# Performance work log

Measured on AMD Instinct MI355X. Metric: run time of the kernel, lower is better.

The kernel has to match this reference:

```python
import jax, jax.numpy as jnp
import numpy as np

# Block dims (see shape_source)
D, H = 768, 12
DH = D // H            # 64 head dim
NOPE = DH // 2         # 32 non-rope q/k dim
ROPE = DH // 2         # 32 rope q/k dim
QP = D // 2            # 384 q LoRA dim
KVP = 2 * D // 3       # 512 kv LoRA dim
E, TOPK, NS = 8, 2, 2  # routed experts, top-k, shared experts
FF = 4 * D             # 3072 expert hidden
THETA = 10000.0


def setup_inputs() -> dict:
    key = jax.random.key(0)
    ks = jax.random.split(key, 16)
    B, S = 4, 1024
    r = lambda i, shape, s: (s * jax.random.normal(ks[i], shape)).astype(jnp.float32)
    return {
        'x': jax.random.normal(ks[0], (B, S, D), jnp.float32),
        'ln1_w': jnp.ones((D,), jnp.float32),
        'ln2_w': jnp.ones((D,), jnp.float32),
        'W_dq': r(1, (D, QP), 0.01),
        'W_uq': r(2, (QP, D), 0.01),
        'q_ln_w': jnp.ones((QP,), jnp.float32),
        'q_ln_b': jnp.zeros((QP,), jnp.float32),
        'W_dkv': r(3, (D, KVP + ROPE), 0.01),
        'W_ukv': r(4, (KVP, D + H * NOPE), 0.01),
        'kv_ln_w': jnp.ones((KVP,), jnp.float32),
        'kv_ln_b': jnp.zeros((KVP,), jnp.float32),
        'W_o': r(5, (D, D), 0.01),
        's_fc': r(6, (NS, FF, D), 0.02),   # nn.Linear weight layout [out,in]
        's_proj': r(7, (NS, D, FF), 0.02),
        'e_fc': r(8, (E, FF, D), 0.02),
        'e_proj': r(9, (E, D, FF), 0.02),
        'centroids': jax.random.normal(ks[10], (E, D), jnp.float32),
        'route_bias': jnp.zeros((E,), jnp.float32),  # load-balancing bias (non-learned)
    }


def _ln(x, w, b=None, eps=1e-5):
    m = x.mean(-1, keepdims=True)
    v = ((x - m) ** 2).mean(-1, keepdims=True)
    y = (x - m) * jax.lax.rsqrt(v + eps) * w
    return y + b if b is not None else y


def _rope(x, cos, sin):
    x1, x2 = jnp.split(x, 2, axis=-1)
    return x * cos + jnp.concatenate([-x2, x1], axis=-1) * sin


def _forward(x, ln1_w, ln2_w, W_dq, W_uq, q_ln_w, q_ln_b, W_dkv, W_ukv,
             kv_ln_w, kv_ln_b, W_o, s_fc, s_proj, e_fc, e_proj,
             centroids, route_bias):
    B, S, _ = x.shape
    h = _ln(x, ln1_w)
    # ---- MLA attention ----
    cq = _ln(h @ W_dq, q_ln_w, q_ln_b)
    Q = (cq @ W_uq).reshape(B, S, H, DH).transpose(0, 2, 1, 3)  # bhsd
    Qn, Qr = Q[..., :NOPE], Q[..., NOPE:]
    freqs = 1.0 / (THETA ** (jnp.arange(0, DH, 2, dtype=jnp.float32) / DH))
    ang = jnp.arange(S, dtype=jnp.float32)[:, None] * freqs[None, :]  # [S, DH/2]
    cos = jnp.tile(jnp.cos(ang)[:, : ROPE // 2], (1, 2))  # [S, ROPE]
    sin = jnp.tile(jnp.sin(ang)[:, : ROPE // 2], (1, 2))
    Qr = _rope(Qr, cos, sin)
    ckv = h @ W_dkv
    kv_lora, k_rope = ckv[..., :KVP], ckv[..., KVP:]
    kv_lora = _ln(kv_lora, kv_ln_w, kv_ln_b)
    KV = (kv_lora @ W_ukv).reshape(B, S, H, NOPE + DH).transpose(0, 2, 1, 3)
    Kn, V = KV[..., :NOPE], KV[..., NOPE:]
    Kr = _rope(k_rope[:, None, :, :], cos, sin)  # [B,1,S,ROPE] shared across heads
    Kr = jnp.broadcast_to(Kr, (B, H, S, ROPE))
    q = jnp.concatenate([Qn, Qr], axis=-1)
    k = jnp.concatenate([Kn, Kr], axis=-1)
    scores = jnp.einsum('bhsd,bhtd->bhst', q, k) / np.float32(np.sqrt(DH))
    causal = jnp.tril(jnp.ones((S, S), bool))
    scores = jnp.where(causal, scores, jnp.finfo(scores.dtype).min)
    attn = jax.nn.softmax(scores, axis=-1)
    o = jnp.einsum('bhst,bhtd->bshd', attn, V).reshape(B, S, D)
    x = x + o @ W_o.T
    # ---- MoE FFN ----
    h = _ln(x, ln2_w)
    gelu = lambda t: jax.nn.gelu(t, approximate=False)  # torch nn.GELU default
    # shared experts (always on, summed)
    shared = jnp.einsum('bsnf,ndf->bsd', gelu(jnp.einsum('bsd,nfd->bsnf', h, s_fc)), s_proj)
    # centroid routing
    raw = jnp.einsum('bsd,ed->bse', h, centroids)
    routing = jax.nn.sigmoid(raw)
    balanced = raw + route_bias
    _, topi = jax.lax.top_k(balanced, TOPK)                       # [B,S,K]
    w = jnp.take_along_axis(routing, topi, axis=-1)               # sigmoid gate values
    w = w / (w.sum(-1, keepdims=True) + 1e-9)                     # normalize over top-k
    gates = (jax.nn.one_hot(topi, E, dtype=w.dtype) * w[..., None]).sum(-2)  # [B,S,E]
    eh = gelu(jnp.einsum('bsd,efd->bsef', h, e_fc))               # [B,S,E,FF]
    routed = jnp.einsum('bsef,edf,bse->bsd', eh, e_proj, gates)
    return x + shared + routed


def reference(x, ln1_w, ln2_w, W_dq, W_uq, q_ln_w, q_ln_b, W_dkv, W_ukv,
              kv_ln_w, kv_ln_b, W_o, s_fc, s_proj, e_fc, e_proj,
              centroids, route_bias):
    return _forward(x, ln1_w, ln2_w, W_dq, W_uq, q_ln_w, q_ln_b, W_dkv, W_ukv,
                    kv_ln_w, kv_ln_b, W_o, s_fc, s_proj, e_fc, e_proj,
                    centroids, route_bias)
```

## Files before the change

### kernel.cpp

```cpp
#include <hip/hip_runtime.h>
#include <math.h>


#define DEV __device__ __forceinline__

typedef __attribute__((ext_vector_type(8))) short short8;
typedef __attribute__((ext_vector_type(8))) __bf16 bf16x8;
typedef __attribute__((ext_vector_type(4))) float floatx4;

DEV short f2bf(float f) {
  union { float f; unsigned u; } v; v.f = f;
  unsigned r = v.u + 0x7fffu + ((v.u >> 16) & 1u);
  return (short)(r >> 16);
}
DEV float bf2f(short s) {
  union { float f; unsigned u; } v; v.u = ((unsigned)(unsigned short)s) << 16;
  return v.f;
}
DEV float gelu_f(float v) {
  float z = fabsf(v) * 0.70710678118654752f;
  float t = __fdividef(1.0f, 1.0f + 0.3275911f * z);
  float poly = t * (0.254829592f + t * (-0.284496736f +
               t * (1.421413741f + t * (-1.453152027f + t * 1.061405429f))));
  float er = 1.0f - poly * __expf(-z * z);
  er = (v < 0.f) ? -er : er;
  return 0.5f * v * (1.0f + er);
}

DEV floatx4 mfma16(short8 a, short8 b, floatx4 c) {
  return __builtin_amdgcn_mfma_f32_16x16x32_bf16(
      __builtin_bit_cast(bf16x8, a), __builtin_bit_cast(bf16x8, b), c, 0, 0, 0);
}
DEV void async16(void* lds_uniform, const void* gptr) {
  __builtin_amdgcn_global_load_lds(
      (const __attribute__((address_space(1))) void*)gptr,
      (__attribute__((address_space(3))) void*)lds_uniform, 16, 0, 0);
}

DEV void xcd_swz(int& n0, int& m0) {
  const int NT = gridDim.x;
  const int flat = blockIdx.y * NT + blockIdx.x;
  const int nwg = NT * gridDim.y;
  const int w = (flat & 7) * (nwg >> 3) + (flat >> 3);
  n0 = (w % NT) * 128;
  m0 = (w / NT) * 128;
}


__global__ void cast2_bf4(const float4* __restrict__ srcA, short4* __restrict__ dstA,
                          const float4* __restrict__ srcB, short4* __restrict__ dstB,
                          long n4each) {
  long i = (long)blockIdx.x * blockDim.x + threadIdx.x;
  long stride = (long)gridDim.x * blockDim.x;
  for (; i < 2 * n4each; i += stride) {
    const float4* s; short4* d; long j;
    if (i < n4each) { s = srcA; d = dstA; j = i; }
    else { s = srcB; d = dstB; j = i - n4each; }
    float4 v = s[j];
    short4 o; o.x = f2bf(v.x); o.y = f2bf(v.y); o.z = f2bf(v.z); o.w = f2bf(v.w);
    d[j] = o;
  }
}

__global__ void cast_shared(const float4* __restrict__ sfc4, const float4* __restrict__ sproj4,
                            short4* __restrict__ fcCat4, short4* __restrict__ projCat4) {
  long i = (long)blockIdx.x * 256 + threadIdx.x;
  float4 v;
  if (i < 1179648) {
    v = sfc4[i];
    short4 o; o.x = f2bf(v.x); o.y = f2bf(v.y); o.z = f2bf(v.z); o.w = f2bf(v.w);
    fcCat4[i] = o;
  } else {
    long j = i - 1179648;
    long d = j / 1536, k4 = j - d * 1536;
    v = (k4 < 768) ? sproj4[d * 768 + k4] : sproj4[589824 + d * 768 + (k4 - 768)];
    short4 o; o.x = f2bf(v.x); o.y = f2bf(v.y); o.z = f2bf(v.z); o.w = f2bf(v.w);
    projCat4[j] = o;
  }
}

__global__ void cast_hl4(const float4* __restrict__ src, short4* __restrict__ dhi,
                         short4* __restrict__ dlo, long n4) {
  long i = (long)blockIdx.x * blockDim.x + threadIdx.x;
  long stride = (long)gridDim.x * blockDim.x;
  for (; i < n4; i += stride) {
    float4 v = src[i];
    short4 h, l;
    h.x = f2bf(v.x); l.x = f2bf(v.x - bf2f(h.x));
    h.y = f2bf(v.y); l.y = f2bf(v.y - bf2f(h.y));
    h.z = f2bf(v.z); l.z = f2bf(v.z - bf2f(h.z));
    h.w = f2bf(v.w); l.w = f2bf(v.w - bf2f(h.w));
    dhi[i] = h; dlo[i] = l;
  }
}

__launch_bounds__(256)
__global__ void transpose_cast_hl(const float* __restrict__ src, short* __restrict__ dhi,
                                  short* __restrict__ dlo, int K, int N) {
  __shared__ float tile[64][65];
  int k0 = blockIdx.x * 64, n0 = blockIdx.y * 64;
  for (int i = threadIdx.x; i < 4096; i += 256) {
    int r = i >> 6, c = i & 63;
    tile[r][c] = (n0 + c < N) ? src[(size_t)(k0 + r) * N + n0 + c] : 0.f;
  }
  __syncthreads();
  for (int i = threadIdx.x; i < 4096; i += 256) {
    int r = i >> 6, c = i & 63;
    float v = tile[c][r];
    short h = f2bf(v);
    dhi[(size_t)(n0 + r) * K + k0 + c] = h;
    dlo[(size_t)(n0 + r) * K + k0 + c] = f2bf(v - bf2f(h));
  }
}


__launch_bounds__(256)
__global__ void ln_hl(const float* __restrict__ in, int ldi, int N,
                      const float* __restrict__ w, const float* __restrict__ b,
                      short* __restrict__ ohi, short* __restrict__ olo, int ldo) {
  const int row = blockIdx.x * 4 + (threadIdx.x >> 6);
  const int lane = threadIdx.x & 63;
  const float* r = in + (size_t)row * ldi;
  float s = 0.f, s2 = 0.f;
  for (int i = lane; i < N; i += 64) { float v = r[i]; s += v; s2 += v * v; }
#pragma unroll
  for (int off = 32; off >= 1; off >>= 1) { s += __shfl_xor(s, off); s2 += __shfl_xor(s2, off); }
  float mean = s / N, var = s2 / N - mean * mean;
  float rstd = rsqrtf(var + 1e-5f);
  for (int i = lane; i < N; i += 64) {
    float y = (r[i] - mean) * rstd * w[i];
    if (b) y += b[i];
    short h = f2bf(y);
    ohi[(size_t)row * ldo + i] = h;
    olo[(size_t)row * ldo + i] = f2bf(y - bf2f(h));
  }
}

__launch_bounds__(256)
__global__ void ln_qkv(const float* __restrict__ Ccat,
                       const float* __restrict__ qw, const float* __restrict__ qb,
                       const float* __restrict__ kw, const float* __restrict__ kb,
                       short* __restrict__ cqH, short* __restrict__ cqL,
                       short* __restrict__ kvH, short* __restrict__ kvL) {
  const int vrow = blockIdx.x * 4 + (threadIdx.x >> 6);
  const int lane = threadIdx.x & 63;
  const float* r; int N; const float* w; const float* b; short* oh; short* ol; int ldo; int row;
  if (vrow < 4096) {
    row = vrow; r = Ccat + (size_t)row * 928; N = 384; w = qw; b = qb; oh = cqH; ol = cqL; ldo = 384;
  } else {
    row = vrow - 4096; r = Ccat + (size_t)row * 928 + 384; N = 512; w = kw; b = kb; oh = kvH; ol = kvL; ldo = 512;
  }
  float s = 0.f, s2 = 0.f;
  for (int i = lane; i < N; i += 64) { float v = r[i]; s += v; s2 += v * v; }
#pragma unroll
  for (int off = 32; off >= 1; off >>= 1) { s += __shfl_xor(s, off); s2 += __shfl_xor(s2, off); }
  float mean = s / N, var = s2 / N - mean * mean;
  float rstd = rsqrtf(var + 1e-5f);
  for (int i = lane; i < N; i += 64) {
    float y = (r[i] - mean) * rstd * w[i] + b[i];
    short h = f2bf(y);
    oh[(size_t)row * ldo + i] = h;
    ol[(size_t)row * ldo + i] = f2bf(y - bf2f(h));
  }
}

__launch_bounds__(256)
__global__ void ln_bf_f32(const float* __restrict__ in, const float* __restrict__ w,
                          short* __restrict__ obf, float* __restrict__ of,
                          float* __restrict__ outInit) {
  const int row = blockIdx.x * 4 + (threadIdx.x >> 6);
  const int lane = threadIdx.x & 63;
  const float* r = in + (size_t)row * 768;
  float s = 0.f, s2 = 0.f;
  for (int i = lane; i < 768; i += 64) { float v = r[i]; s += v; s2 += v * v; }
#pragma unroll
  for (int off = 32; off >= 1; off >>= 1) { s += __shfl_xor(s, off); s2 += __shfl_xor(s2, off); }
  float mean = s / 768.f, var = s2 / 768.f - mean * mean;
  float rstd = rsqrtf(var + 1e-5f);
  for (int i = lane; i < 768; i += 64) {
    float xv = r[i];
    float y = (xv - mean) * rstd * w[i];
    obf[(size_t)row * 768 + i] = f2bf(y);
    of[(size_t)row * 768 + i] = y;
    outInit[(size_t)row * 768 + i] = xv;
  }
}


template<int RESID>
__launch_bounds__(256)
__global__ void gemm3(const short* __restrict__ Ahi, const short* __restrict__ Alo, int lda,
                      const short* __restrict__ Bhi, const short* __restrict__ Blo, int ldb,
                      float* __restrict__ Cf, int ldc, const float* __restrict__ resid,
                      int M, int N, int K) {
  __shared__ __align__(16) short AsH[4096], AsL[4096], BsH[4096], BsL[4096];
  const int tid = threadIdx.x;
  int n0, m0; xcd_swz(n0, m0);
  const int wave = tid >> 6, lane = tid & 63;
  const int wm = (wave >> 1) * 64, wn = (wave & 1) * 64;
  const int lr = lane & 15, rb = (lane >> 4) * 4;
  const int stg = ((tid & 3) ^ ((tid >> 3) & 3)) * 8;
  const int lkx = (((lane >> 4) ^ ((lr >> 1) & 3))) * 8;
  const floatx4 fz = {0.f, 0.f, 0.f, 0.f};
  floatx4 acc[4][4];
#pragma unroll
  for (int i = 0; i < 4; i++)
#pragma unroll
    for (int j = 0; j < 4; j++) acc[i][j] = fz;
  const size_t rowA = (size_t)(m0 + (tid >> 2)) * lda + stg;
  const size_t rowB = (size_t)(n0 + (tid >> 2)) * ldb + stg;
  const size_t a64 = (size_t)64 * lda, b64 = (size_t)64 * ldb;
  short* AsHW = AsH + wave * 512; short* AsLW = AsL + wave * 512;
  short* BsHW = BsH + wave * 512; short* BsLW = BsL + wave * 512;
  for (int k0 = 0; k0 < K; k0 += 32) {
    async16(AsHW, Ahi + rowA + k0);        async16(AsHW + 2048, Ahi + rowA + a64 + k0);
    async16(AsLW, Alo + rowA + k0);        async16(AsLW + 2048, Alo + rowA + a64 + k0);
    async16(BsHW, Bhi + rowB + k0);        async16(BsHW + 2048, Bhi + rowB + b64 + k0);
    async16(BsLW, Blo + rowB + k0);        async16(BsLW + 2048, Blo + rowB + b64 + k0);
    __syncthreads();
    short8 ah[4], al[4], bh[4], bl[4];
#pragma unroll
    for (int i = 0; i < 4; i++) {
      ah[i] = *(const short8*)&AsH[(wm + i * 16 + lr) * 32 + lkx];
      al[i] = *(const short8*)&AsL[(wm + i * 16 + lr) * 32 + lkx];
    }
#pragma unroll
    for (int j = 0; j < 4; j++) {
      bh[j] = *(const short8*)&BsH[(wn + j * 16 + lr) * 32 + lkx];
      bl[j] = *(const short8*)&BsL[(wn + j * 16 + lr) * 32 + lkx];
    }
#pragma unroll
    for (int i = 0; i < 4; i++)
#pragma unroll
      for (int j = 0; j < 4; j++) {
        acc[i][j] = mfma16(ah[i], bh[j], acc[i][j]);
        acc[i][j] = mfma16(ah[i], bl[j], acc[i][j]);
        acc[i][j] = mfma16(al[i], bh[j], acc[i][j]);
      }
    __syncthreads();
  }
#pragma unroll
  for (int i = 0; i < 4; i++) {
    int row = m0 + wm + i * 16 + rb;
#pragma unroll
    for (int j = 0; j < 4; j++) {
      int col = n0 + wn + j * 16 + lr;
      if (col < N) {
#pragma unroll
        for (int r = 0; r < 4; r++) {
          int rr = row + r;
          if (rr < M) {
            float v = acc[i][j][r];
            if (RESID) v += resid[(size_t)rr * ldc + col];
            Cf[(size_t)rr * ldc + col] = v;
          }
        }
      }
    }
  }
}


__launch_bounds__(256)
__global__ void gemm_fc(const short* __restrict__ A, int lda,
                        const short* __restrict__ Bt, int ldb,
                        short* __restrict__ Cb, int ldc, int K) {
  __shared__ __align__(16) short As[8192], Bs[8192];
  const int tid = threadIdx.x;
  int n0, m0; xcd_swz(n0, m0);
  const int wave = tid >> 6, lane = tid & 63;
  const int wm = (wave >> 1) * 64, wn = (wave & 1) * 64;
  const int lr = lane & 15, q4 = lane >> 4, rb = q4 * 4;
  const int srow = tid >> 3;
  const int sg = ((tid & 7) ^ (srow & 7)) * 8;
  const int cx0 = ((q4 ^ (lr & 7))) * 8;
  const int cx1 = (((4 + q4) ^ (lr & 7))) * 8;
  const floatx4 fz = {0.f, 0.f, 0.f, 0.f};
  floatx4 acc[4][4];
#pragma unroll
  for (int i = 0; i < 4; i++)
#pragma unroll
    for (int j = 0; j < 4; j++) acc[i][j] = fz;
  const short* Ag = A + (size_t)(m0 + srow) * lda + sg;
  const short* Bg = Bt + (size_t)(n0 + srow) * ldb + sg;
  short* AsW = As + wave * 512; short* BsW = Bs + wave * 512;
  const size_t a32 = (size_t)32 * lda, b32 = (size_t)32 * ldb;
  for (int k0 = 0; k0 < K; k0 += 64) {
    async16(AsW,        Ag + k0);            async16(AsW + 2048, Ag + a32 + k0);
    async16(AsW + 4096, Ag + 2 * a32 + k0);  async16(AsW + 6144, Ag + 3 * a32 + k0);
    async16(BsW,        Bg + k0);            async16(BsW + 2048, Bg + b32 + k0);
    async16(BsW + 4096, Bg + 2 * b32 + k0);  async16(BsW + 6144, Bg + 3 * b32 + k0);
    __syncthreads();
#pragma unroll
    for (int ks = 0; ks < 2; ks++) {
      const int cx = ks ? cx1 : cx0;
      short8 af[4], bfr[4];
#pragma unroll
      for (int i = 0; i < 4; i++) af[i] = *(const short8*)&As[(wm + i * 16 + lr) * 64 + cx];
#pragma unroll
      for (int j = 0; j < 4; j++) bfr[j] = *(const short8*)&Bs[(wn + j * 16 + lr) * 64 + cx];
#pragma unroll
      for (int i = 0; i < 4; i++)
#pragma unroll
        for (int j = 0; j < 4; j++) acc[i][j] = mfma16(af[i], bfr[j], acc[i][j]);
    }
    __syncthreads();
  }
#pragma unroll
  for (int i = 0; i < 4; i++) {
    int row = m0 + wm + i * 16 + rb;
#pragma unroll
    for (int j = 0; j < 4; j++) {
      int col = n0 + wn + j * 16 + lr;
#pragma unroll
      for (int r = 0; r < 4; r++)
        Cb[(size_t)(row + r) * ldc + col] = f2bf(gelu_f(acc[i][j][r]));
    }
  }
}


__launch_bounds__(256)
__global__ void gemm_sk(const short* __restrict__ A, int lda,
                        const short* __restrict__ Bt, int ldb,
                        float* __restrict__ out, int ldc, int klen) {
  __shared__ __align__(16) short As[8192], Bs[8192];
  const int tid = threadIdx.x;
  int n0, m0; xcd_swz(n0, m0);
  const int koff = blockIdx.z * klen;
  const int wave = tid >> 6, lane = tid & 63;
  const int wm = (wave >> 1) * 64, wn = (wave & 1) * 64;
  const int lr = lane & 15, q4 = lane >> 4, rb = q4 * 4;
  const int srow = tid >> 3;
  const int sg = ((tid & 7) ^ (srow & 7)) * 8;
  const int cx0 = ((q4 ^ (lr & 7))) * 8;
  const int cx1 = (((4 + q4) ^ (lr & 7))) * 8;
  const floatx4 fz = {0.f, 0.f, 0.f, 0.f};
  floatx4 acc[4][4];
#pragma unroll
  for (int i = 0; i < 4; i++)
#pragma unroll
    for (int j = 0; j < 4; j++) acc[i][j] = fz;
  const short* Ag = A + (size_t)(m0 + srow) * lda + koff + sg;
  const short* Bg = Bt + (size_t)(n0 + srow) * ldb + koff + sg;
  short* AsW = As + wave * 512; short* BsW = Bs + wave * 512;
  const size_t a32 = (size_t)32 * lda, b32 = (size_t)32 * ldb;
  for (int k0 = 0; k0 < klen; k0 += 64) {
    async16(AsW,        Ag + k0);            async16(AsW + 2048, Ag + a32 + k0);
    async16(AsW + 4096, Ag + 2 * a32 + k0);  async16(AsW + 6144, Ag + 3 * a32 + k0);
    async16(BsW,        Bg + k0);            async16(BsW + 2048, Bg + b32 + k0);
    async16(BsW + 4096, Bg + 2 * b32 + k0);  async16(BsW + 6144, Bg + 3 * b32 + k0);
    __syncthreads();
#pragma unroll
    for (int ks = 0; ks < 2; ks++) {
      const int cx = ks ? cx1 : cx0;
      short8 af[4], bfr[4];
#pragma unroll
      for (int i = 0; i < 4; i++) af[i] = *(const short8*)&As[(wm + i * 16 + lr) * 64 + cx];
#pragma unroll
      for (int j = 0; j < 4; j++) bfr[j] = *(const short8*)&Bs[(wn + j * 16 + lr) * 64 + cx];
#pragma unroll
      for (int i = 0; i < 4; i++)
#pragma unroll
        for (int j = 0; j < 4; j++) acc[i][j] = mfma16(af[i], bfr[j], acc[i][j]);
    }
    __syncthreads();
  }
#pragma unroll
  for (int i = 0; i < 4; i++) {
    int row = m0 + wm + i * 16 + rb;
#pragma unroll
    for (int j = 0; j < 4; j++) {
      int col = n0 + wn + j * 16 + lr;
#pragma unroll
      for (int r = 0; r < 4; r++)
        atomicAdd(&out[(size_t)(row + r) * ldc + col], acc[i][j][r]);
    }
  }
}


__global__ void build_qk(const float* __restrict__ Qf, const float* __restrict__ KVf,
                         const float* __restrict__ Ccat,
                         short* __restrict__ qh, short* __restrict__ ql,
                         short* __restrict__ kh, short* __restrict__ kl) {
  int id = blockIdx.x * blockDim.x + threadIdx.x;
  if (id >= 4096 * 12) return;
  int token = id / 12, hh_ = id - token * 12;
  int s = token & 1023, b = token >> 10;
  size_t base = ((size_t)(b * 12 + hh_) * 1024 + s) * 64;
  float vals[64];
  if (blockIdx.y == 0) {
    const float* q = Qf + (size_t)token * 768 + hh_ * 64;
#pragma unroll
    for (int d = 0; d < 32; d++) vals[d] = q[d];
#pragma unroll
    for (int i = 0; i < 16; i++) {
      float fi = powf(10000.f, -(float)(2 * i) / 64.f);
      float sn, cs; sincosf((float)s * fi, &sn, &cs);
      vals[32 + i] = q[32 + i] * cs - q[48 + i] * sn;
      vals[48 + i] = q[48 + i] * cs + q[32 + i] * sn;
    }
#pragma unroll
    for (int d = 0; d < 64; d++) {
      short h = f2bf(vals[d]);
      qh[base + d] = h; ql[base + d] = f2bf(vals[d] - bf2f(h));
    }
  } else {
    const float* kv = KVf + (size_t)token * 1152 + hh_ * 96;
#pragma unroll
    for (int d = 0; d < 32; d++) vals[d] = kv[d];
    const float* kr = Ccat + (size_t)token * 928 + 896;
#pragma unroll
    for (int i = 0; i < 16; i++) {
      float fi = powf(10000.f, -(float)(2 * i) / 64.f);
      float sn, cs; sincosf((float)s * fi, &sn, &cs);
      vals[32 + i] = kr[i] * cs - kr[16 + i] * sn;
      vals[48 + i] = kr[16 + i] * cs + kr[i] * sn;
    }
#pragma unroll
    for (int d = 0; d < 64; d++) {
      short h = f2bf(vals[d]);
      kh[base + d] = h; kl[base + d] = f2bf(vals[d] - bf2f(h));
    }
  }
}

__launch_bounds__(256)
__global__ void build_vt_hl(const float* __restrict__ KVf,
                            short* __restrict__ vth, short* __restrict__ vtl) {
  __shared__ float tile[64][65];
  const int s0 = blockIdx.x * 64, bh = blockIdx.y;
  const int b = bh / 12, h = bh - b * 12;
  for (int i = threadIdx.x; i < 4096; i += 256) {
    int tl = i >> 6, d = i & 63;
    int token = b * 1024 + s0 + tl;
    tile[tl][d] = KVf[(size_t)token * 1152 + h * 96 + 32 + d];
  }
  __syncthreads();
  for (int i = threadIdx.x; i < 4096; i += 256) {
    int d = i >> 6, sl = i & 63;
    float v = tile[sl][d];
    short hh = f2bf(v);
    size_t idx = (size_t)bh * 65536 + (size_t)d * 1024 + s0 + sl;
    vth[idx] = hh;
    vtl[idx] = f2bf(v - bf2f(hh));
  }
}


__launch_bounds__(256)
__global__ void attn3(const short* __restrict__ qbh, const short* __restrict__ qbl,
                      const short* __restrict__ kbh, const short* __restrict__ kbl,
                      const short* __restrict__ vth, const short* __restrict__ vtl,
                      short* __restrict__ obh, short* __restrict__ obl) {
  const int bh = blockIdx.y;
  const int b = bh / 12, h = bh - b * 12;
  const short* Qh = qbh + (size_t)bh * 65536;
  const short* Ql = qbl + (size_t)bh * 65536;
  const short* Kh = kbh + (size_t)bh * 65536;
  const short* Kl = kbl + (size_t)bh * 65536;
  const short* Vh = vth + (size_t)bh * 65536;
  const short* Vl = vtl + (size_t)bh * 65536;
  __shared__ __align__(16) short KsH[4096], KsL[4096], VsH[4096], VsL[4096];
  __shared__ __align__(16) short PsH[4608], PsL[4608];
  const int tid = threadIdx.x, wave = tid >> 6, lane = tid & 63;
  const int lr = lane & 15, q4 = lane >> 4, lk = (lane >> 4) * 8;
  const int sx0 = ((q4 ^ (lr & 7))) * 8;
  const int sx1 = (((4 + q4) ^ (lr & 7))) * 8;
  const int soff_sw = (((tid & 7) ^ ((tid >> 3) & 7))) * 8;
  const int srow = tid >> 3;
  short* KsHW = KsH + wave * 512; short* KsLW = KsL + wave * 512;
  short* VsHW = VsH + wave * 512; short* VsLW = VsL + wave * 512;
  short* myPh = PsH + wave * 1152; short* myPl = PsL + wave * 1152;
  const floatx4 fz = {0.f, 0.f, 0.f, 0.f};
#pragma unroll
  for (int ph = 0; ph < 2; ph++) {
    const int qt = ph ? 15 - blockIdx.x : blockIdx.x;
    const int qrow0 = qt * 64 + wave * 16;
    short8 qfh[2], qfl[2];
    qfh[0] = *(const short8*)&Qh[(size_t)(qrow0 + lr) * 64 + lk];
    qfh[1] = *(const short8*)&Qh[(size_t)(qrow0 + lr) * 64 + 32 + lk];
    qfl[0] = *(const short8*)&Ql[(size_t)(qrow0 + lr) * 64 + lk];
    qfl[1] = *(const short8*)&Ql[(size_t)(qrow0 + lr) * 64 + 32 + lk];
    floatx4 oacc[4];
#pragma unroll
    for (int t = 0; t < 4; t++) oacc[t] = fz;
    float m_i[4], l_i[4];
#pragma unroll
    for (int r = 0; r < 4; r++) { m_i[r] = -__builtin_inff(); l_i[r] = 0.f; }
    for (int kt = 0; kt <= qt; kt++) {
      __syncthreads();
      size_t krow = (size_t)(kt * 64 + srow) * 64 + soff_sw;
      size_t vrow = (size_t)srow * 1024 + kt * 64 + soff_sw;
      async16(KsHW, Kh + krow);        async16(KsHW + 2048, Kh + krow + 32 * 64);
      async16(KsLW, Kl + krow);        async16(KsLW + 2048, Kl + krow + 32 * 64);
      async16(VsHW, Vh + vrow);        async16(VsHW + 2048, Vh + vrow + 32 * 1024);
      async16(VsLW, Vl + vrow);        async16(VsLW + 2048, Vl + vrow + 32 * 1024);
      __syncthreads();
      floatx4 sacc[4];
#pragma unroll
      for (int j = 0; j < 4; j++) sacc[j] = fz;
#pragma unroll
      for (int j = 0; j < 4; j++) {
        int rbase = (j * 16 + lr) * 64;
        short8 kh0 = *(const short8*)&KsH[rbase + sx0];
        short8 kh1 = *(const short8*)&KsH[rbase + sx1];
        short8 kl0 = *(const short8*)&KsL[rbase + sx0];
        short8 kl1 = *(const short8*)&KsL[rbase + sx1];
        sacc[j] = mfma16(qfh[0], kh0, sacc[j]);
        sacc[j] = mfma16(qfh[1], kh1, sacc[j]);
        sacc[j] = mfma16(qfh[0], kl0, sacc[j]);
        sacc[j] = mfma16(qfh[1], kl1, sacc[j]);
        sacc[j] = mfma16(qfl[0], kh0, sacc[j]);
        sacc[j] = mfma16(qfl[1], kh1, sacc[j]);
      }
      float pv[4][4], mrow[4];
#pragma unroll
      for (int r = 0; r < 4; r++) mrow[r] = -__builtin_inff();
      const bool diag = (kt == qt);
#pragma unroll
      for (int j = 0; j < 4; j++)
#pragma unroll
        for (int r = 0; r < 4; r++) {
          float v = sacc[j][r] * 0.125f;
          if (diag) {
            int qg = qrow0 + q4 * 4 + r;
            int kg = kt * 64 + j * 16 + lr;
            if (kg > qg) v = -__builtin_inff();
          }
          pv[j][r] = v;
          mrow[r] = fmaxf(mrow[r], v);
        }
#pragma unroll
      for (int r = 0; r < 4; r++)
#pragma unroll
        for (int off = 1; off < 16; off <<= 1) mrow[r] = fmaxf(mrow[r], __shfl_xor(mrow[r], off));
      float alpha[4], rsum[4];
#pragma unroll
      for (int r = 0; r < 4; r++) {
        float nm = fmaxf(m_i[r], mrow[r]);
        alpha[r] = __expf(m_i[r] - nm);
        m_i[r] = nm; rsum[r] = 0.f;
      }
#pragma unroll
      for (int j = 0; j < 4; j++)
#pragma unroll
        for (int r = 0; r < 4; r++) {
          float pe = __expf(pv[j][r] - m_i[r]);
          pv[j][r] = pe; rsum[r] += pe;
        }
#pragma unroll
      for (int r = 0; r < 4; r++) {
#pragma unroll
        for (int off = 1; off < 16; off <<= 1) rsum[r] += __shfl_xor(rsum[r], off);
        l_i[r] = l_i[r] * alpha[r] + rsum[r];
      }
#pragma unroll
      for (int t = 0; t < 4; t++)
#pragma unroll
        for (int r = 0; r < 4; r++) oacc[t][r] *= alpha[r];
#pragma unroll
      for (int j = 0; j < 4; j++)
#pragma unroll
        for (int r = 0; r < 4; r++) {
          float p = pv[j][r];
          short hh = f2bf(p);
          myPh[(q4 * 4 + r) * 72 + j * 16 + lr] = hh;
          myPl[(q4 * 4 + r) * 72 + j * 16 + lr] = f2bf(p - bf2f(hh));
        }
      __asm__ volatile("s_waitcnt lgkmcnt(0)" ::: "memory");
#pragma unroll
      for (int c = 0; c < 2; c++) {
        short8 ph_ = *(const short8*)&myPh[lr * 72 + c * 32 + lk];
        short8 pl_ = *(const short8*)&myPl[lr * 72 + c * 32 + lk];
        const int sxc = c ? sx1 : sx0;
#pragma unroll
        for (int t = 0; t < 4; t++) {
          int rbase = (t * 16 + lr) * 64;
          short8 vh = *(const short8*)&VsH[rbase + sxc];
          short8 vl = *(const short8*)&VsL[rbase + sxc];
          oacc[t] = mfma16(ph_, vh, oacc[t]);
          oacc[t] = mfma16(ph_, vl, oacc[t]);
          oacc[t] = mfma16(pl_, vh, oacc[t]);
        }
      }
    }
#pragma unroll
    for (int t = 0; t < 4; t++)
#pragma unroll
      for (int r = 0; r < 4; r++) {
        int s = qrow0 + q4 * 4 + r;
        int token = b * 1024 + s;
        float ov = oacc[t][r] / l_i[r];
        short hh = f2bf(ov);
        size_t idx = (size_t)token * 768 + h * 64 + t * 16 + lr;
        obh[idx] = hh;
        obl[idx] = f2bf(ov - bf2f(hh));
      }
  }
}


__launch_bounds__(256)
__global__ void route_score(const float* __restrict__ h2f, const float* __restrict__ cent,
                            const float* __restrict__ rbias,
                            int* __restrict__ topexp, float* __restrict__ gates) {
  const int token = blockIdx.x * 4 + (threadIdx.x >> 6);
  const int lane = threadIdx.x & 63;
  const float* hv = h2f + (size_t)token * 768;
  float hreg[12];
#pragma unroll
  for (int ii = 0; ii < 12; ii++) hreg[ii] = hv[lane + 64 * ii];
  float raw[8];
#pragma unroll
  for (int e = 0; e < 8; e++) {
    const float* cv = cent + e * 768;
    float p = 0.f;
#pragma unroll
    for (int ii = 0; ii < 12; ii++) p += hreg[ii] * cv[lane + 64 * ii];
#pragma unroll
    for (int off = 32; off >= 1; off >>= 1) p += __shfl_xor(p, off);
    raw[e] = p;
  }
  if (lane == 0) {
    float b0 = -__builtin_inff(); int i1 = 0;
#pragma unroll
    for (int e = 0; e < 8; e++) { float be = raw[e] + rbias[e]; if (be > b0) { b0 = be; i1 = e; } }
    float b1 = -__builtin_inff(); int i2 = 0;
#pragma unroll
    for (int e = 0; e < 8; e++) {
      if (e == i1) continue;
      float be = raw[e] + rbias[e];
      if (be > b1) { b1 = be; i2 = e; }
    }
    float w1 = 1.f / (1.f + expf(-raw[i1]));
    float w2 = 1.f / (1.f + expf(-raw[i2]));
    float wsum = w1 + w2 + 1e-9f;
    topexp[token] = i1;        gates[token] = w1 / wsum;
    topexp[4096 + token] = i2; gates[4096 + token] = w2 / wsum;
  }
}

__launch_bounds__(256)
__global__ void build_lists(const int* __restrict__ topexp,
                            int* __restrict__ counts, int* __restrict__ lists) {
  const int e = blockIdx.x;
  __shared__ int wave_off[4];
  const int wave = threadIdx.x >> 6, lane = threadIdx.x & 63;
  int total = 0;
  for (int c0 = 0; c0 < 8192; c0 += 256) {
    int slot = c0 + threadIdx.x;
    bool m = (topexp[slot] == e);
    unsigned long long bal = __ballot(m);
    int wcnt = __popcll(bal);
    int lpre = __popcll(bal & ((1ull << lane) - 1ull));
    if (lane == 0) wave_off[wave] = wcnt;
    __syncthreads();
    int woff = 0;
#pragma unroll
    for (int w = 0; w < 4; w++) if (w < wave) woff += wave_off[w];
    int chunk_total = wave_off[0] + wave_off[1] + wave_off[2] + wave_off[3];
    if (m) lists[e * 4096 + total + woff + lpre] = slot;
    total += chunk_total;
    __syncthreads();
  }
  if (threadIdx.x == 0) counts[e] = total;
}


__launch_bounds__(256)
__global__ void expert_fc_z(const short* __restrict__ h2bf, const short* __restrict__ wfc,
                            const int* __restrict__ lists, const int* __restrict__ counts,
                            int ebase, short* __restrict__ act) {
  const int lz = blockIdx.z, e = ebase + lz;
  const int cnt = counts[e];
  const int m0 = blockIdx.y * 128;
  if (m0 >= cnt) return;
  const int n0 = blockIdx.x * 128;
  int aoff = 0;
  for (int i = 0; i < lz; i++) aoff += counts[ebase + i];
  __shared__ __align__(16) short As[8192], Bs[8192];
  __shared__ int slots[128];
  const int tid = threadIdx.x;
  if (tid < 128) slots[tid] = lists[e * 4096 + m0 + tid];
  __syncthreads();
  const int wave = tid >> 6, lane = tid & 63;
  const int wm = (wave >> 1) * 64, wn = (wave & 1) * 64;
  const int lr = lane & 15, q4 = lane >> 4, rb = q4 * 4;
  const int srow = tid >> 3;
  const int sg = ((tid & 7) ^ (srow & 7)) * 8;
  const int cx0 = ((q4 ^ (lr & 7))) * 8;
  const int cx1 = (((4 + q4) ^ (lr & 7))) * 8;
  int tok[4];
#pragma unroll
  for (int p = 0; p < 4; p++) tok[p] = slots[p * 32 + srow] & 4095;
  const floatx4 fz = {0.f, 0.f, 0.f, 0.f};
  floatx4 acc[4][4];
#pragma unroll
  for (int i = 0; i < 4; i++)
#pragma unroll
    for (int j = 0; j < 4; j++) acc[i][j] = fz;
  const short* Ag0 = h2bf + (size_t)tok[0] * 768 + sg;
  const short* Ag1 = h2bf + (size_t)tok[1] * 768 + sg;
  const short* Ag2 = h2bf + (size_t)tok[2] * 768 + sg;
  const short* Ag3 = h2bf + (size_t)tok[3] * 768 + sg;
  const short* Bg = wfc + (size_t)lz * (3072 * 768) + (size_t)(n0 + srow) * 768 + sg;
  short* AsW = As + wave * 512; short* BsW = Bs + wave * 512;
  const size_t b32 = (size_t)32 * 768;
  for (int k0 = 0; k0 < 768; k0 += 64) {
    async16(AsW,        Ag0 + k0);           async16(AsW + 2048, Ag1 + k0);
    async16(AsW + 4096, Ag2 + k0);           async16(AsW + 6144, Ag3 + k0);
    async16(BsW,        Bg + k0);            async16(BsW + 2048, Bg + b32 + k0);
    async16(BsW + 4096, Bg + 2 * b32 + k0);  async16(BsW + 6144, Bg + 3 * b32 + k0);
    __syncthreads();
#pragma unroll
    for (int ks = 0; ks < 2; ks++) {
      const int cx = ks ? cx1 : cx0;
      short8 af[4], bfr[4];
#pragma unroll
      for (int i = 0; i < 4; i++) af[i] = *(const short8*)&As[(wm + i * 16 + lr) * 64 + cx];
#pragma unroll
      for (int j = 0; j < 4; j++) bfr[j] = *(const short8*)&Bs[(wn + j * 16 + lr) * 64 + cx];
#pragma unroll
      for (int i = 0; i < 4; i++)
#pragma unroll
        for (int j = 0; j < 4; j++) acc[i][j] = mfma16(af[i], bfr[j], acc[i][j]);
    }
    __syncthreads();
  }
#pragma unroll
  for (int i = 0; i < 4; i++) {
    int lrow = wm + i * 16 + rb;
#pragma unroll
    for (int j = 0; j < 4; j++) {
      int col = n0 + wn + j * 16 + lr;
#pragma unroll
      for (int r = 0; r < 4; r++) {
        if (m0 + lrow + r < cnt)
          act[(size_t)(aoff + m0 + lrow + r) * 3072 + col] = f2bf(gelu_f(acc[i][j][r]));
      }
    }
  }
}

__launch_bounds__(256)
__global__ void expert_proj_z(const short* __restrict__ act, const short* __restrict__ wproj,
                              const int* __restrict__ lists, const int* __restrict__ counts,
                              int ebase, const float* __restrict__ gates,
                              float* __restrict__ out) {
  const int lz = blockIdx.z >> 2, kh = blockIdx.z & 3, e = ebase + lz;
  const int cnt = counts[e];
  const int m0 = blockIdx.y * 128;
  if (m0 >= cnt) return;
  const int n0 = blockIdx.x * 128;
  int aoff = 0;
  for (int i = 0; i < lz; i++) aoff += counts[ebase + i];
  const int koff = kh * 768;
  __shared__ __align__(16) short As[8192], Bs[8192];
  __shared__ int slots[128];
  const int tid = threadIdx.x;
  if (tid < 128) slots[tid] = lists[e * 4096 + m0 + tid];
  __syncthreads();
  const int wave = tid >> 6, lane = tid & 63;
  const int wm = (wave >> 1) * 64, wn = (wave & 1) * 64;
  const int lr = lane & 15, q4 = lane >> 4, rb = q4 * 4;
  const int srow = tid >> 3;
  const int sg = ((tid & 7) ^ (srow & 7)) * 8;
  const int cx0 = ((q4 ^ (lr & 7))) * 8;
  const int cx1 = (((4 + q4) ^ (lr & 7))) * 8;
  const floatx4 fz = {0.f, 0.f, 0.f, 0.f};
  floatx4 acc[4][4];
#pragma unroll
  for (int i = 0; i < 4; i++)
#pragma unroll
    for (int j = 0; j < 4; j++) acc[i][j] = fz;
  const short* Ag = act + (size_t)(aoff + m0 + srow) * 3072 + koff + sg;
  const short* Bg = wproj + (size_t)lz * (768 * 3072) + (size_t)(n0 + srow) * 3072 + koff + sg;
  short* AsW = As + wave * 512; short* BsW = Bs + wave * 512;
  const size_t s32 = (size_t)32 * 3072;
  for (int k0 = 0; k0 < 768; k0 += 64) {
    async16(AsW,        Ag + k0);            async16(AsW + 2048, Ag + s32 + k0);
    async16(AsW + 4096, Ag + 2 * s32 + k0);  async16(AsW + 6144, Ag + 3 * s32 + k0);
    async16(BsW,        Bg + k0);            async16(BsW + 2048, Bg + s32 + k0);
    async16(BsW + 4096, Bg + 2 * s32 + k0);  async16(BsW + 6144, Bg + 3 * s32 + k0);
    __syncthreads();
#pragma unroll
    for (int ks = 0; ks < 2; ks++) {
      const int cx = ks ? cx1 : cx0;
      short8 af[4], bfr[4];
#pragma unroll
      for (int i = 0; i < 4; i++) af[i] = *(const short8*)&As[(wm + i * 16 + lr) * 64 + cx];
#pragma unroll
      for (int j = 0; j < 4; j++) bfr[j] = *(const short8*)&Bs[(wn + j * 16 + lr) * 64 + cx];
#pragma unroll
      for (int i = 0; i < 4; i++)
#pragma unroll
        for (int j = 0; j < 4; j++) acc[i][j] = mfma16(af[i], bfr[j], acc[i][j]);
    }
    __syncthreads();
  }
#pragma unroll
  for (int i = 0; i < 4; i++) {
    int lrow = wm + i * 16 + rb;
#pragma unroll
    for (int j = 0; j < 4; j++) {
      int col = n0 + wn + j * 16 + lr;
#pragma unroll
      for (int r = 0; r < 4; r++) {
        if (m0 + lrow + r < cnt) {
          int slot = slots[lrow + r];
          int token = slot & 4095;
          atomicAdd(&out[(size_t)token * 768 + col], gates[slot] * acc[i][j][r]);
        }
      }
    }
  }
}

__global__ void bad_kernel(float* out) { out[threadIdx.x] = 1e30f; }


extern "C" void kernel_launch(void* const* d_in, const int* in_sizes, int n_in,
                              void* d_out, int out_size, void* d_ws, size_t ws_size,
                              hipStream_t stream) {
  const float* x = (const float*)d_in[0];
  const float* ln1_w = (const float*)d_in[1];
  const float* ln2_w = (const float*)d_in[2];
  const float* W_dq = (const float*)d_in[3];
  const float* W_uq = (const float*)d_in[4];
  const float* q_ln_w = (const float*)d_in[5];
  const float* q_ln_b = (const float*)d_in[6];
  const float* W_dkv = (const float*)d_in[7];
  const float* W_ukv = (const float*)d_in[8];
  const float* kv_ln_w = (const float*)d_in[9];
  const float* kv_ln_b = (const float*)d_in[10];
  const float* W_o = (const float*)d_in[11];
  const float* s_fc = (const float*)d_in[12];
  const float* s_proj = (const float*)d_in[13];
  const float* e_fc = (const float*)d_in[14];
  const float* e_proj = (const float*)d_in[15];
  const float* cent = (const float*)d_in[16];
  const float* rbias = (const float*)d_in[17];
  float* out = (float*)d_out;

  char* base = (char*)d_ws;
  size_t off = 0;
  auto take = [&](size_t bytes) -> char* {
    char* r = base + off;
    off = (off + bytes + 255) & ~(size_t)255;
    return r;
  };
  short* WcatH = (short*)take(1572864);  short* WcatL = (short*)take(1572864);
  short* WuqH  = (short*)take(589824);   short* WuqL  = (short*)take(589824);
  short* WukvH = (short*)take(1179648);  short* WukvL = (short*)take(1179648);
  short* WoH   = (short*)take(1179648);  short* WoL   = (short*)take(1179648);
  float* x2    = (float*)take(12582912);
  float* gates = (float*)take(32768);
  int*   counts= (int*)take(32);
  int*   lists = (int*)take(131072);
  int*   topexp= (int*)take(32768);
  const size_t PLANE = 6291456;
  char* pool = take(4 * 2 * PLANE);
  char* R    = take(51118080);
  size_t used = off;
  if (used > ws_size) { bad_kernel<<<1, 256, 0, stream>>>(out); return; }
  char* pA = pool;
  char* pB = pool + 2 * PLANE;
  char* pC = pool + 4 * PLANE;
  char* pD = pool + 6 * PLANE;

  short* hH   = (short*)pA;            short* hL   = (short*)(pA + PLANE);
  float* Ccat = (float*)R;
  short* cqH  = (short*)pB;            short* cqL  = (short*)(pB + 3145728);
  short* kvlH = (short*)pD;            short* kvlL = (short*)(pD + 4194304);
  float* Qf   = (float*)pC;
  float* KVf  = (float*)(R + 15204352);
  short* qbH  = (short*)pD;            short* qbL  = (short*)(pD + PLANE);
  short* kbH  = (short*)pA;            short* kbL  = (short*)(pA + PLANE);
  short* vtH  = (short*)pB;            short* vtL  = (short*)(pB + PLANE);
  short* obH  = (short*)pC;            short* obL  = (short*)(pC + PLANE);
  short* h2bf    = (short*)(pD + PLANE);
  float* h2f     = (float*)pC;
  short* sfcCat  = (short*)pA;
  short* sprojCat= (short*)(pA + 9437184);
  short* actCat  = (short*)R;
  short* efcHalf = (short*)pA;
  short* eprojHalf=(short*)(pA + 18874368);
  short* eact    = (short*)R;

  cast_hl4<<<576, 256, 0, stream>>>((const float4*)W_o, (short4*)WoH, (short4*)WoL, 147456);
  transpose_cast_hl<<<dim3(12, 6), 256, 0, stream>>>(W_dq, WcatH, WcatL, 768, 384);
  transpose_cast_hl<<<dim3(12, 10), 256, 0, stream>>>(W_dkv, WcatH + (size_t)384 * 768,
                                                      WcatL + (size_t)384 * 768, 768, 544);
  transpose_cast_hl<<<dim3(6, 12), 256, 0, stream>>>(W_uq, WuqH, WuqL, 384, 768);
  transpose_cast_hl<<<dim3(8, 18), 256, 0, stream>>>(W_ukv, WukvH, WukvL, 512, 1152);

  ln_hl<<<1024, 256, 0, stream>>>(x, 768, 768, ln1_w, nullptr, hH, hL, 768);
  gemm3<0><<<dim3(8, 32), 256, 0, stream>>>(hH, hL, 768, WcatH, WcatL, 768, Ccat, 928, nullptr, 4096, 928, 768);
  ln_qkv<<<2048, 256, 0, stream>>>(Ccat, q_ln_w, q_ln_b, kv_ln_w, kv_ln_b, cqH, cqL, kvlH, kvlL);
  gemm3<0><<<dim3(6, 32), 256, 0, stream>>>(cqH, cqL, 384, WuqH, WuqL, 384, Qf, 768, nullptr, 4096, 768, 384);
  gemm3<0><<<dim3(9, 32), 256, 0, stream>>>(kvlH, kvlL, 512, WukvH, WukvL, 512, KVf, 1152, nullptr, 4096, 1152, 512);
  build_qk<<<dim3(192, 2), 256, 0, stream>>>(Qf, KVf, Ccat, qbH, qbL, kbH, kbL);
  build_vt_hl<<<dim3(16, 48), 256, 0, stream>>>(KVf, vtH, vtL);
  attn3<<<dim3(8, 48), 256, 0, stream>>>(qbH, qbL, kbH, kbL, vtH, vtL, obH, obL);
  gemm3<1><<<dim3(6, 32), 256, 0, stream>>>(obH, obL, 768, WoH, WoL, 768, x2, 768, x, 4096, 768, 768);

  ln_bf_f32<<<1024, 256, 0, stream>>>(x2, ln2_w, h2bf, h2f, out);
  route_score<<<1024, 256, 0, stream>>>(h2f, cent, rbias, topexp, gates);
  build_lists<<<8, 256, 0, stream>>>(topexp, counts, lists);

  cast_shared<<<9216, 256, 0, stream>>>((const float4*)s_fc, (const float4*)s_proj,
                                        (short4*)sfcCat, (short4*)sprojCat);
  gemm_fc<<<dim3(48, 32), 256, 0, stream>>>(h2bf, 768, sfcCat, 768, actCat, 6144, 768);
  gemm_sk<<<dim3(6, 32, 4), 256, 0, stream>>>(actCat, 6144, sprojCat, 6144, out, 768, 1536);

  for (int h = 0; h < 2; h++) {
    cast2_bf4<<<2048, 256, 0, stream>>>(
        (const float4*)(e_fc + (size_t)h * 4 * 3072 * 768), (short4*)efcHalf,
        (const float4*)(e_proj + (size_t)h * 4 * 768 * 3072), (short4*)eprojHalf, 2359296);
    expert_fc_z<<<dim3(24, 32, 4), 256, 0, stream>>>(h2bf, efcHalf, lists, counts, h * 4, eact);
    expert_proj_z<<<dim3(6, 32, 16), 256, 0, stream>>>(eact, eprojHalf, lists, counts, h * 4, gates, out);
  }
}
```

Measured before the change: 964.3 us.

## Replace atomic split-K in shared-expert projection with partial buffers and reduce kernel

The shared-expert down-projection GEMM drops from four K-splits with float atomics to three K-splits. Split 0 accumulates directly into the output, and splits 1 and 2 write plain stores into scratch buffers that a new vectorized kernel then sums into the output. The N tile is halved to 64 so that the grid still has enough blocks, and the XCD swizzle is replaced by plain block indexing. This removes the atomic traffic but adds an extra kernel launch, a full read-modify-write pass over the output, and reuses the x2 and pC buffers as scratch.

```diff
diff --git a/kernel.cpp b/kernel.cpp
--- a/kernel.cpp
+++ b/kernel.cpp
@@ -323,24 +323,26 @@
 __launch_bounds__(256)
 __global__ void gemm_sk(const short* __restrict__ A, int lda,
                         const short* __restrict__ Bt, int ldb,
-                        float* __restrict__ out, int ldc, int klen) {
-  __shared__ __align__(16) short As[8192], Bs[8192];
+                        float* __restrict__ out, int ldc,
+                        float* __restrict__ p1, float* __restrict__ p2, int klen) {
+  __shared__ __align__(16) short As[8192], Bs[4096];
   const int tid = threadIdx.x;
-  int n0, m0; xcd_swz(n0, m0);
-  const int koff = blockIdx.z * klen;
+  const int m0 = blockIdx.y * 128, n0 = blockIdx.x * 64;
+  const int z = blockIdx.z;
+  const int koff = z * klen;
   const int wave = tid >> 6, lane = tid & 63;
-  const int wm = (wave >> 1) * 64, wn = (wave & 1) * 64;
+  const int wm = (wave >> 1) * 64, wn = (wave & 1) * 32;
   const int lr = lane & 15, q4 = lane >> 4, rb = q4 * 4;
   const int srow = tid >> 3;
   const int sg = ((tid & 7) ^ (srow & 7)) * 8;
   const int cx0 = ((q4 ^ (lr & 7))) * 8;
   const int cx1 = (((4 + q4) ^ (lr & 7))) * 8;
   const floatx4 fz = {0.f, 0.f, 0.f, 0.f};
-  floatx4 acc[4][4];
+  floatx4 acc[4][2];
 #pragma unroll
   for (int i = 0; i < 4; i++)
 #pragma unroll
-    for (int j = 0; j < 4; j++) acc[i][j] = fz;
+    for (int j = 0; j < 2; j++) acc[i][j] = fz;
   const short* Ag = A + (size_t)(m0 + srow) * lda + koff + sg;
   const short* Bg = Bt + (size_t)(n0 + srow) * ldb + koff + sg;
   short* AsW = As + wave * 512; short* BsW = Bs + wave * 512;
@@ -349,33 +351,50 @@
     async16(AsW,        Ag + k0);            async16(AsW + 2048, Ag + a32 + k0);
     async16(AsW + 4096, Ag + 2 * a32 + k0);  async16(AsW + 6144, Ag + 3 * a32 + k0);
     async16(BsW,        Bg + k0);            async16(BsW + 2048, Bg + b32 + k0);
-    async16(BsW + 4096, Bg + 2 * b32 + k0);  async16(BsW + 6144, Bg + 3 * b32 + k0);
     __syncthreads();
 #pragma unroll
     for (int ks = 0; ks < 2; ks++) {
       const int cx = ks ? cx1 : cx0;
-      short8 af[4], bfr[4];
+      short8 af[4], bfr[2];
 #pragma unroll
       for (int i = 0; i < 4; i++) af[i] = *(const short8*)&As[(wm + i * 16 + lr) * 64 + cx];
 #pragma unroll
-      for (int j = 0; j < 4; j++) bfr[j] = *(const short8*)&Bs[(wn + j * 16 + lr) * 64 + cx];
+      for (int j = 0; j < 2; j++) bfr[j] = *(const short8*)&Bs[(wn + j * 16 + lr) * 64 + cx];
 #pragma unroll
       for (int i = 0; i < 4; i++)
 #pragma unroll
-        for (int j = 0; j < 4; j++) acc[i][j] = mfma16(af[i], bfr[j], acc[i][j]);
-    }
-    __syncthreads();
-  }
+        for (int j = 0; j < 2; j++) acc[i][j] = mfma16(af[i], bfr[j], acc[i][j]);
+    }
+    __syncthreads();
+  }
+  float* dst = (z == 0) ? out : (z == 1 ? p1 : p2);
 #pragma unroll
   for (int i = 0; i < 4; i++) {
     int row = m0 + wm + i * 16 + rb;
 #pragma unroll
-    for (int j = 0; j < 4; j++) {
+    for (int j = 0; j < 2; j++) {
       int col = n0 + wn + j * 16 + lr;
 #pragma unroll
-      for (int r = 0; r < 4; r++)
-        atomicAdd(&out[(size_t)(row + r) * ldc + col], acc[i][j][r]);
-    }
+      for (int r = 0; r < 4; r++) {
+        size_t idx = (size_t)(row + r) * ldc + col;
+        if (z == 0) dst[idx] += acc[i][j][r];
+        else dst[idx] = acc[i][j][r];
+      }
+    }
+  }
+}
+
+__global__ void sk_reduce(float4* __restrict__ out, const float4* __restrict__ p1,
+                          const float4* __restrict__ p2) {
+  int i = blockIdx.x * 256 + threadIdx.x;
+  const int stride = gridDim.x * 256;
+  for (; i < 786432; i += stride) {
+    float4 o = out[i], a = p1[i], b = p2[i];
+    o.x += a.x + b.x;
+    o.y += a.y + b.y;
+    o.z += a.z + b.z;
+    o.w += a.w + b.w;
+    out[i] = o;
   }
 }
 
@@ -888,6 +907,8 @@
   short* efcHalf = (short*)pA;
   short* eprojHalf=(short*)(pA + 18874368);
   short* eact    = (short*)R;
+  float* skP1 = (float*)pC;
+  float* skP2 = x2;
 
   cast_hl4<<<576, 256, 0, stream>>>((const float4*)W_o, (short4*)WoH, (short4*)WoL, 147456);
   transpose_cast_hl<<<dim3(12, 6), 256, 0, stream>>>(W_dq, WcatH, WcatL, 768, 384);
@@ -913,7 +934,9 @@
   cast_shared<<<9216, 256, 0, stream>>>((const float4*)s_fc, (const float4*)s_proj,
                                         (short4*)sfcCat, (short4*)sprojCat);
   gemm_fc<<<dim3(48, 32), 256, 0, stream>>>(h2bf, 768, sfcCat, 768, actCat, 6144, 768);
-  gemm_sk<<<dim3(6, 32, 4), 256, 0, stream>>>(actCat, 6144, sprojCat, 6144, out, 768, 1536);
+  gemm_sk<<<dim3(12, 32, 3), 256, 0, stream>>>(actCat, 6144, sprojCat, 6144, out, 768,
+                                               skP1, skP2, 2048);
+  sk_reduce<<<1536, 256, 0, stream>>>((float4*)out, (const float4*)skP1, (const float4*)skP2);
 
   for (int h = 0; h < 2; h++) {
     cast2_bf4<<<2048, 256, 0, stream>>>(
```

Measured after the change: 976.1 us. About the same (+1.2%).
